# Kernel tuning notes

Hardware: AMD Instinct MI355X
Metric: run time of the kernel (lower is better)

Reference implementation:

```python
import jax, jax.numpy as jnp
import numpy as np

B, N, D = 4096, 32768, 1024

def _l2norm(x, eps=1e-12):
    # matches F.normalize(p=2, dim=-1): x / max(||x||, eps)
    n = jnp.sqrt(jnp.sum(x * x, axis=-1, keepdims=True))
    return x / jnp.maximum(n, eps)

def setup_inputs() -> dict:
    key = jax.random.key(0)
    k1, k2, k3 = jax.random.split(key, 3)
    return {
        "query": jax.random.normal(k1, (B, D), dtype=jnp.float32),
        "keys": jax.random.normal(k2, (N, D), dtype=jnp.float32),
        "values": jax.random.normal(k3, (N, D), dtype=jnp.float32),
    }

def reference(query, keys, values):
    q = _l2norm(query.astype(jnp.float32))          # [B, D]
    k = _l2norm(keys.astype(jnp.float32))           # [N, D]
    v = values.astype(jnp.float32)                  # [N, Dv]
    sim = jnp.einsum('bd,nd->bn', q, k)             # [B, N] cosine similarities
    # torch .var(dim=-1) is unbiased (ddof=1)
    attention_var = jnp.var(sim, axis=-1, ddof=1).mean()
    best = jnp.argmax(sim, axis=-1)                 # [B]
    retrieved = v[best]                             # [B, Dv] gather
    return retrieved, attention_var
```

## Files before the change

### kernel.cpp

```cpp
#include <hip/hip_runtime.h>
#include <math.h>
#include <stdint.h>

#define B_ 4096
#define N_ 32768
#define D_ 1024

#define BM 128
#define BN 128
#define NT 2
#define NCHUNK 128
#define KTOT 32

typedef __attribute__((ext_vector_type(8))) short short8;
typedef __attribute__((ext_vector_type(4))) float f4;
typedef unsigned short u16;

__device__ __forceinline__ u16 bf16_rn(float x) {
    uint32_t u = __float_as_uint(x);
    u += 0x7fffu + ((u >> 16) & 1u);
    return (u16)(u >> 16);
}

__device__ __forceinline__ void split4(f4 v, uint2& hpack, uint2& lpack) {
    u16 h[4], l[4];
    #pragma unroll
    for (int e = 0; e < 4; ++e) {
        float x = v[e];
        u16 hb = bf16_rn(x);
        float hf = __uint_as_float(((uint32_t)hb) << 16);
        h[e] = hb;
        l[e] = bf16_rn(x - hf);
    }
    hpack.x = (uint32_t)h[0] | ((uint32_t)h[1] << 16);
    hpack.y = (uint32_t)h[2] | ((uint32_t)h[3] << 16);
    lpack.x = (uint32_t)l[0] | ((uint32_t)l[1] << 16);
    lpack.y = (uint32_t)l[2] | ((uint32_t)l[3] << 16);
}

__device__ __forceinline__ void g2l16(const void* g, void* l) {
    __builtin_amdgcn_global_load_lds(
        (const __attribute__((address_space(1))) char*)(uintptr_t)g,
        (__attribute__((address_space(3))) char*)(uint32_t)(uintptr_t)l,
        16, 0, 0);
}

__global__ __launch_bounds__(256) void norm_kernel(
    const float* __restrict__ q, const float* __restrict__ k,
    float* __restrict__ invq, float* __restrict__ invk,
    float* __restrict__ out)
{
    const int row = blockIdx.x;
    const int t = threadIdx.x;

    const float* src;
    float* dst;
    if (row < B_) { src = q + (size_t)row * D_;          dst = invq + row; }
    else          { src = k + (size_t)(row - B_) * D_;   dst = invk + (row - B_); }

    float4 v = ((const float4*)src)[t];
    float s = v.x * v.x + v.y * v.y + v.z * v.z + v.w * v.w;

    #pragma unroll
    for (int off = 32; off > 0; off >>= 1)
        s += __shfl_down(s, off);

    __shared__ float red[4];
    if ((t & 63) == 0) red[t >> 6] = s;
    __syncthreads();
    if (t == 0) {
        float tot = red[0] + red[1] + red[2] + red[3];
        *dst = 1.0f / fmaxf(sqrtf(tot), 1e-12f);
        if (row == 0) out[(size_t)B_ * D_] = 0.0f;
    }
}

__global__ __launch_bounds__(256) void split_pack_kernel(
    const float* __restrict__ q, const float* __restrict__ k,
    const float* __restrict__ invq, const float* __restrict__ invk,
    u16* __restrict__ qhi, u16* __restrict__ qlo,
    u16* __restrict__ khi, u16* __restrict__ klo)
{
    const int g = blockIdx.x;
    const int lane = threadIdx.x & 63;
    const int w = threadIdx.x >> 6;

    const float* src; const float* inv;
    u16 *dhi, *dlo; int groups, gg;
    if (g < B_ / 16) { src = q; inv = invq; dhi = qhi; dlo = qlo; groups = B_ / 16; gg = g; }
    else { src = k; inv = invk; dhi = khi; dlo = klo; groups = N_ / 16; gg = g - B_ / 16; }

    const int row = gg * 16 + (lane & 15);
    const float scale = inv[row];
    const int kofs = (lane >> 4) * 8;
    const float* rp = src + (size_t)row * D_;

    #pragma unroll 1
    for (int kt = w; kt < KTOT; kt += 4) {
        f4 v0 = *(const f4*)(rp + kt * 32 + kofs);
        f4 v1 = *(const f4*)(rp + kt * 32 + kofs + 4);
        v0 *= scale; v1 *= scale;
        uint2 h0, l0, h1, l1;
        split4(v0, h0, l0);
        split4(v1, h1, l1);
        const size_t cbase = ((size_t)kt * groups + gg) * 512 + lane * 8;
        uint4 hh = {h0.x, h0.y, h1.x, h1.y};
        uint4 ll = {l0.x, l0.y, l1.x, l1.y};
        *(uint4*)(dhi + cbase) = hh;
        *(uint4*)(dlo + cbase) = ll;
    }
}

__global__ __launch_bounds__(256) void sim_stats_kernel(
    const u16* __restrict__ qhi, const u16* __restrict__ qlo,
    const u16* __restrict__ khi, const u16* __restrict__ klo,
    float* __restrict__ partials)
{
    __shared__ __align__(16) char smem[65536];

    const int tid = threadIdx.x;
    const int lane = tid & 63;
    const int w = tid >> 6;
    const int wm = w >> 1, wn = w & 1;
    const int quad = lane >> 4;
    const int l16 = lane & 15;
    const int mtile = blockIdx.x;
    const int chunk = blockIdx.y;
    const int b0 = mtile * BM;

    const u16* sbase = (w == 0) ? qhi : (w == 1) ? qlo : (w == 2) ? khi : klo;
    const int groups = (w < 2) ? (B_ / 16) : (N_ / 16);

    float (*scan)[68] = (float(*)[68])smem;

    float r_sum = 0.f, r_sq = 0.f, r_m1 = -INFINITY, r_m2 = -INFINITY;
    int r_i1 = 0x7fffffff, r_i2 = 0x7fffffff;

    const f4 zf = {0.f, 0.f, 0.f, 0.f};

    for (int nt = 0; nt < NT; ++nt) {
        const int n0 = chunk * (BN * NT) + nt * BN;
        const int g0 = ((w < 2) ? b0 : n0) >> 4;

        __syncthreads();
        {
            const size_t cb = ((size_t)0 * groups + g0) * 512 + lane * 8;
            char* dst = smem + w * 8192;
            #pragma unroll
            for (int t = 0; t < 8; ++t)
                g2l16(sbase + cb + t * 512, dst + t * 1024);
        }

        f4 acc[4][4];
        #pragma unroll
        for (int i = 0; i < 4; ++i)
            #pragma unroll
            for (int j = 0; j < 4; ++j) acc[i][j] = zf;

        for (int kt = 0; kt < KTOT; ++kt) {
            const int cur = kt & 1;
            __syncthreads();
            if (kt + 1 < KTOT) {
                const size_t cb = ((size_t)(kt + 1) * groups + g0) * 512 + lane * 8;
                char* dst = smem + (1 - cur) * 32768 + w * 8192;
                #pragma unroll
                for (int t = 0; t < 8; ++t)
                    g2l16(sbase + cb + t * 512, dst + t * 1024);
            }
            const char* cbuf = smem + cur * 32768;

            short8 ah[4], al[4];
            #pragma unroll
            for (int i = 0; i < 4; ++i) {
                ah[i] = *(const short8*)(cbuf + (wm * 4 + i) * 1024 + lane * 16);
                al[i] = *(const short8*)(cbuf + 8192 + (wm * 4 + i) * 1024 + lane * 16);
            }
            #pragma unroll
            for (int j = 0; j < 4; ++j) {
                short8 bh = *(const short8*)(cbuf + 16384 + (wn * 4 + j) * 1024 + lane * 16);
                short8 bl = *(const short8*)(cbuf + 24576 + (wn * 4 + j) * 1024 + lane * 16);
                #pragma unroll
                for (int i = 0; i < 4; ++i) {
                    acc[i][j] = __builtin_amdgcn_mfma_f32_16x16x32_bf16(ah[i], bh, acc[i][j], 0, 0, 0);
                    acc[i][j] = __builtin_amdgcn_mfma_f32_16x16x32_bf16(ah[i], bl, acc[i][j], 0, 0, 0);
                    acc[i][j] = __builtin_amdgcn_mfma_f32_16x16x32_bf16(al[i], bh, acc[i][j], 0, 0, 0);
                }
            }
        }

        const int srow = tid >> 1;
        const int c0 = (tid & 1) * 32;
        #pragma unroll 1
        for (int h = 0; h < 2; ++h) {
            __syncthreads();
            if (wn == h) {
                #pragma unroll
                for (int i = 0; i < 4; ++i)
                    #pragma unroll
                    for (int j = 0; j < 4; ++j)
                        #pragma unroll
                        for (int p = 0; p < 4; ++p)
                            scan[wm*64 + i*16 + quad*4 + p][j*16 + l16] = acc[i][j][p];
            }
            __syncthreads();
            const int gbase = n0 + h * 64 + c0;
            #pragma unroll
            for (int u = 0; u < 8; ++u) {
                const f4 v = *(const f4*)&scan[srow][c0 + 4*u];
                #pragma unroll
                for (int e = 0; e < 4; ++e) {
                    const float sv = v[e];
                    const int gi = gbase + 4*u + e;
                    r_sum += sv;
                    r_sq = fmaf(sv, sv, r_sq);
                    if (sv > r_m1)      { r_m2 = r_m1; r_i2 = r_i1; r_m1 = sv; r_i1 = gi; }
                    else if (sv > r_m2) { r_m2 = sv; r_i2 = gi; }
                }
            }
        }
    }

    __syncthreads();
    float* mb = (float*)smem;
    mb[tid*6+0] = r_sum; mb[tid*6+1] = r_sq;
    mb[tid*6+2] = r_m1;  mb[tid*6+3] = __int_as_float(r_i1);
    mb[tid*6+4] = r_m2;  mb[tid*6+5] = __int_as_float(r_i2);
    __syncthreads();
    if ((tid & 1) == 0) {
        const float* o = mb + (size_t)(tid + 1) * 6;
        const float bs = o[0], bq = o[1], bm1 = o[2], bm2 = o[4];
        const int bi1 = __float_as_int(o[3]), bi2 = __float_as_int(o[5]);
        float s = r_sum + bs, q2 = r_sq + bq;
        float m1 = r_m1, m2 = r_m2; int i1 = r_i1, i2 = r_i2;
        if (bm1 > m1 || (bm1 == m1 && bi1 < i1)) {
            float nm2; int ni2;
            if (m1 > bm2 || (m1 == bm2 && i1 < bi2)) { nm2 = m1; ni2 = i1; }
            else                                     { nm2 = bm2; ni2 = bi2; }
            m1 = bm1; i1 = bi1; m2 = nm2; i2 = ni2;
        } else if (bm1 > m2 || (bm1 == m2 && bi1 < i2)) {
            m2 = bm1; i2 = bi1;
        }
        const int row = b0 + (tid >> 1);
        float* p = partials + ((size_t)row * NCHUNK + chunk) * 8;
        f4 p0 = {s, q2, m1, __int_as_float(i1)};
        f4 p1 = {m2, __int_as_float(i2), 0.f, 0.f};
        *(f4*)p = p0;
        *(f4*)(p + 4) = p1;
    }
}

__global__ __launch_bounds__(64) void finalize_kernel(
    const float* __restrict__ partials,
    const float* __restrict__ qg, const float* __restrict__ kg,
    const float* __restrict__ values,
    const float* __restrict__ invq, const float* __restrict__ invk,
    float* __restrict__ out)
{
    const int b = blockIdx.x;
    const int lane = threadIdx.x;

    float s = 0.f, q2 = 0.f, m1 = -INFINITY, m2 = -INFINITY;
    int i1 = 0x7fffffff, i2 = 0x7fffffff;
    #pragma unroll
    for (int cc = 0; cc < NCHUNK / 64; ++cc) {
        const int c = lane + cc * 64;
        const float* p = partials + ((size_t)b * NCHUNK + c) * 8;
        const float bs = p[0], bq = p[1], bm1 = p[2], bm2 = p[4];
        const int bi1 = __float_as_int(p[3]), bi2 = __float_as_int(p[5]);
        s += bs; q2 += bq;
        if (bm1 > m1 || (bm1 == m1 && bi1 < i1)) {
            float nm2; int ni2;
            if (m1 > bm2 || (m1 == bm2 && i1 < bi2)) { nm2 = m1; ni2 = i1; }
            else                                     { nm2 = bm2; ni2 = bi2; }
            m1 = bm1; i1 = bi1; m2 = nm2; i2 = ni2;
        } else if (bm1 > m2 || (bm1 == m2 && bi1 < i2)) {
            m2 = bm1; i2 = bi1;
        }
    }
    #pragma unroll
    for (int msk = 1; msk < 64; msk <<= 1) {
        const float bs = __shfl_xor(s, msk), bq = __shfl_xor(q2, msk);
        const float bm1 = __shfl_xor(m1, msk), bm2 = __shfl_xor(m2, msk);
        const int bi1 = __shfl_xor(i1, msk), bi2 = __shfl_xor(i2, msk);
        s += bs; q2 += bq;
        if (bm1 > m1 || (bm1 == m1 && bi1 < i1)) {
            float nm2; int ni2;
            if (m1 > bm2 || (m1 == bm2 && i1 < bi2)) { nm2 = m1; ni2 = i1; }
            else                                     { nm2 = bm2; ni2 = bi2; }
            m1 = bm1; i1 = bi1; m2 = nm2; i2 = ni2;
        } else if (bm1 > m2 || (bm1 == m2 && bi1 < i2)) {
            m2 = bm1; i2 = bi1;
        }
    }
    if (lane == 0) {
        const float var = (q2 - s * s / (float)N_) / (float)(N_ - 1);
        atomicAdd(out + (size_t)B_ * D_, var * (1.0f / B_));
    }

    const float* qrow = qg + (size_t)b * D_;
    const float* k1 = kg + (size_t)i1 * D_;
    const float* k2 = kg + (size_t)i2 * D_;
    double d1 = 0.0, d2 = 0.0;
    #pragma unroll
    for (int v4 = 0; v4 < 4; ++v4) {
        const int off = v4 * 256 + lane * 4;
        const f4 qv = *(const f4*)(qrow + off);
        const f4 a1 = *(const f4*)(k1 + off);
        const f4 a2 = *(const f4*)(k2 + off);
        #pragma unroll
        for (int e = 0; e < 4; ++e) {
            d1 += (double)qv[e] * (double)a1[e];
            d2 += (double)qv[e] * (double)a2[e];
        }
    }
    #pragma unroll
    for (int msk = 1; msk < 64; msk <<= 1) {
        d1 += __shfl_xor(d1, msk);
        d2 += __shfl_xor(d2, msk);
    }
    const double sc = (double)invq[b];
    const double s1 = d1 * sc * (double)invk[i1];
    const double s2 = d2 * sc * (double)invk[i2];
    const int winner = (s2 > s1 || (s2 == s1 && i2 < i1)) ? i2 : i1;

    const float* vrow = values + (size_t)winner * D_;
    float* orow = out + (size_t)b * D_;
    #pragma unroll
    for (int v4 = 0; v4 < 4; ++v4) {
        const int off = v4 * 256 + lane * 4;
        *(f4*)(orow + off) = *(const f4*)(vrow + off);
    }
}

extern "C" void kernel_launch(void* const* d_in, const int* in_sizes, int n_in,
                              void* d_out, int out_size, void* d_ws, size_t ws_size,
                              hipStream_t stream)
{
    const float* q = (const float*)d_in[0];
    const float* k = (const float*)d_in[1];
    const float* v = (const float*)d_in[2];
    float* out = (float*)d_out;
    float* ws = (float*)d_ws;

    float* invq = ws;
    float* invk = ws + B_;
    float* partials = ws + B_ + N_;
    u16* qhi = (u16*)(partials + (size_t)B_ * NCHUNK * 8);
    u16* qlo = qhi + (size_t)B_ * D_;
    u16* khi = qlo + (size_t)B_ * D_;
    u16* klo = khi + (size_t)N_ * D_;

    norm_kernel<<<B_ + N_, 256, 0, stream>>>(q, k, invq, invk, out);
    split_pack_kernel<<<(B_ + N_) / 16, 256, 0, stream>>>(q, k, invq, invk, qhi, qlo, khi, klo);
    sim_stats_kernel<<<dim3(B_ / BM, NCHUNK), 256, 0, stream>>>(qhi, qlo, khi, klo, partials);
    finalize_kernel<<<B_, 64, 0, stream>>>(partials, q, k, v, invq, invk, out);
}
```

Measured before the change: 1.006 ms.

## Fuse norm into pack kernel and load Q fragments directly from global

Merges the row-norm kernel into the split/pack kernel so each row is read once and one launch disappears. In the similarity kernel, the A (query) fragments are now loaded straight from global memory into registers instead of being staged through LDS. This halves the shared-memory buffer and adds a launch-bounds occupancy hint of 4 blocks. The risk is exposed global-load latency on the A operand each k-step, since only B stays double-buffered.

```diff
diff --git a/kernel.cpp b/kernel.cpp
--- a/kernel.cpp
+++ b/kernel.cpp
@@ -11,6 +11,8 @@
 #define NT 2
 #define NCHUNK 128
 #define KTOT 32
+#define QG (B_ / 16)
+#define KG (N_ / 16)
 
 typedef __attribute__((ext_vector_type(8))) short short8;
 typedef __attribute__((ext_vector_type(4))) float f4;
@@ -45,78 +47,71 @@
         16, 0, 0);
 }
 
-__global__ __launch_bounds__(256) void norm_kernel(
+__global__ __launch_bounds__(256) void pack_kernel(
     const float* __restrict__ q, const float* __restrict__ k,
     float* __restrict__ invq, float* __restrict__ invk,
+    u16* __restrict__ qhi, u16* __restrict__ qlo,
+    u16* __restrict__ khi, u16* __restrict__ klo,
     float* __restrict__ out)
-{
-    const int row = blockIdx.x;
-    const int t = threadIdx.x;
-
-    const float* src;
-    float* dst;
-    if (row < B_) { src = q + (size_t)row * D_;          dst = invq + row; }
-    else          { src = k + (size_t)(row - B_) * D_;   dst = invk + (row - B_); }
-
-    float4 v = ((const float4*)src)[t];
-    float s = v.x * v.x + v.y * v.y + v.z * v.z + v.w * v.w;
-
-    #pragma unroll
-    for (int off = 32; off > 0; off >>= 1)
-        s += __shfl_down(s, off);
-
-    __shared__ float red[4];
-    if ((t & 63) == 0) red[t >> 6] = s;
-    __syncthreads();
-    if (t == 0) {
-        float tot = red[0] + red[1] + red[2] + red[3];
-        *dst = 1.0f / fmaxf(sqrtf(tot), 1e-12f);
-        if (row == 0) out[(size_t)B_ * D_] = 0.0f;
-    }
-}
-
-__global__ __launch_bounds__(256) void split_pack_kernel(
-    const float* __restrict__ q, const float* __restrict__ k,
-    const float* __restrict__ invq, const float* __restrict__ invk,
-    u16* __restrict__ qhi, u16* __restrict__ qlo,
-    u16* __restrict__ khi, u16* __restrict__ klo)
 {
     const int g = blockIdx.x;
     const int lane = threadIdx.x & 63;
     const int w = threadIdx.x >> 6;
 
-    const float* src; const float* inv;
+    const float* src; float* invdst;
     u16 *dhi, *dlo; int groups, gg;
-    if (g < B_ / 16) { src = q; inv = invq; dhi = qhi; dlo = qlo; groups = B_ / 16; gg = g; }
-    else { src = k; inv = invk; dhi = khi; dlo = klo; groups = N_ / 16; gg = g - B_ / 16; }
+    if (g < B_ / 16) { src = q; invdst = invq; dhi = qhi; dlo = qlo; groups = QG; gg = g; }
+    else { src = k; invdst = invk; dhi = khi; dlo = klo; groups = KG; gg = g - B_ / 16; }
 
     const int row = gg * 16 + (lane & 15);
-    const float scale = inv[row];
     const int kofs = (lane >> 4) * 8;
     const float* rp = src + (size_t)row * D_;
 
-    #pragma unroll 1
-    for (int kt = w; kt < KTOT; kt += 4) {
-        f4 v0 = *(const f4*)(rp + kt * 32 + kofs);
-        f4 v1 = *(const f4*)(rp + kt * 32 + kofs + 4);
-        v0 *= scale; v1 *= scale;
+    f4 v0[8], v1[8];
+    float s = 0.f;
+    #pragma unroll
+    for (int u = 0; u < 8; ++u) {
+        const int kt = w + u * 4;
+        v0[u] = *(const f4*)(rp + kt * 32 + kofs);
+        v1[u] = *(const f4*)(rp + kt * 32 + kofs + 4);
+        #pragma unroll
+        for (int e = 0; e < 4; ++e) {
+            s = fmaf(v0[u][e], v0[u][e], s);
+            s = fmaf(v1[u][e], v1[u][e], s);
+        }
+    }
+    s += __shfl_xor(s, 16);
+    s += __shfl_xor(s, 32);
+    __shared__ float red[4][16];
+    if ((lane >> 4) == 0) red[w][lane & 15] = s;
+    __syncthreads();
+    const float tot = red[0][lane & 15] + red[1][lane & 15]
+                    + red[2][lane & 15] + red[3][lane & 15];
+    const float scale = 1.0f / fmaxf(sqrtf(tot), 1e-12f);
+    if (w == 0 && lane < 16) invdst[gg * 16 + lane] = scale;
+
+    #pragma unroll
+    for (int u = 0; u < 8; ++u) {
+        const int kt = w + u * 4;
+        f4 a = v0[u] * scale, b = v1[u] * scale;
         uint2 h0, l0, h1, l1;
-        split4(v0, h0, l0);
-        split4(v1, h1, l1);
+        split4(a, h0, l0);
+        split4(b, h1, l1);
         const size_t cbase = ((size_t)kt * groups + gg) * 512 + lane * 8;
         uint4 hh = {h0.x, h0.y, h1.x, h1.y};
         uint4 ll = {l0.x, l0.y, l1.x, l1.y};
         *(uint4*)(dhi + cbase) = hh;
         *(uint4*)(dlo + cbase) = ll;
     }
-}
-
-__global__ __launch_bounds__(256) void sim_stats_kernel(
+    if (g == 0 && threadIdx.x == 0) out[(size_t)B_ * D_] = 0.0f;
+}
+
+__global__ __launch_bounds__(256, 4) void sim_stats_kernel(
     const u16* __restrict__ qhi, const u16* __restrict__ qlo,
     const u16* __restrict__ khi, const u16* __restrict__ klo,
     float* __restrict__ partials)
 {
-    __shared__ __align__(16) char smem[65536];
+    __shared__ __align__(16) char smem[34816];
 
     const int tid = threadIdx.x;
     const int lane = tid & 63;
@@ -128,8 +123,11 @@
     const int chunk = blockIdx.y;
     const int b0 = mtile * BM;
 
-    const u16* sbase = (w == 0) ? qhi : (w == 1) ? qlo : (w == 2) ? khi : klo;
-    const int groups = (w < 2) ? (B_ / 16) : (N_ / 16);
+    const int aG0 = (b0 >> 4) + wm * 4;
+    const int plane = w >> 1;
+    const u16* __restrict__ kbase = plane ? klo : khi;
+    const int sub0 = (w & 1) * 4;
+    char* const dst0 = smem + plane * 8192 + sub0 * 1024;
 
     float (*scan)[68] = (float(*)[68])smem;
 
@@ -140,15 +138,14 @@
 
     for (int nt = 0; nt < NT; ++nt) {
         const int n0 = chunk * (BN * NT) + nt * BN;
-        const int g0 = ((w < 2) ? b0 : n0) >> 4;
+        const int g0 = n0 >> 4;
 
         __syncthreads();
         {
-            const size_t cb = ((size_t)0 * groups + g0) * 512 + lane * 8;
-            char* dst = smem + w * 8192;
+            const size_t cb = ((size_t)(g0 + sub0)) * 512 + lane * 8;
             #pragma unroll
-            for (int t = 0; t < 8; ++t)
-                g2l16(sbase + cb + t * 512, dst + t * 1024);
+            for (int t = 0; t < 4; ++t)
+                g2l16(kbase + cb + t * 512, dst0 + t * 1024);
         }
 
         f4 acc[4][4];
@@ -160,25 +157,30 @@
         for (int kt = 0; kt < KTOT; ++kt) {
             const int cur = kt & 1;
             __syncthreads();
+
+            short8 ah[4], al[4];
+            {
+                const size_t ab = ((size_t)kt * QG + aG0) * 512 + lane * 8;
+                #pragma unroll
+                for (int i = 0; i < 4; ++i) {
+                    ah[i] = *(const short8*)(qhi + ab + i * 512);
+                    al[i] = *(const short8*)(qlo + ab + i * 512);
+                }
+            }
+
             if (kt + 1 < KTOT) {
-                const size_t cb = ((size_t)(kt + 1) * groups + g0) * 512 + lane * 8;
-                char* dst = smem + (1 - cur) * 32768 + w * 8192;
-                #pragma unroll
-                for (int t = 0; t < 8; ++t)
-                    g2l16(sbase + cb + t * 512, dst + t * 1024);
-            }
-            const char* cbuf = smem + cur * 32768;
-
-            short8 ah[4], al[4];
-            #pragma unroll
-            for (int i = 0; i < 4; ++i) {
-                ah[i] = *(const short8*)(cbuf + (wm * 4 + i) * 1024 + lane * 16);
-                al[i] = *(const short8*)(cbuf + 8192 + (wm * 4 + i) * 1024 + lane * 16);
-            }
+                const size_t cb = ((size_t)(kt + 1) * KG + g0 + sub0) * 512 + lane * 8;
+                char* dst = smem + (1 - cur) * 16384 + plane * 8192 + sub0 * 1024;
+                #pragma unroll
+                for (int t = 0; t < 4; ++t)
+                    g2l16(kbase + cb + t * 512, dst + t * 1024);
+            }
+
+            const char* cbuf = smem + cur * 16384;
             #pragma unroll
             for (int j = 0; j < 4; ++j) {
-                short8 bh = *(const short8*)(cbuf + 16384 + (wn * 4 + j) * 1024 + lane * 16);
-                short8 bl = *(const short8*)(cbuf + 24576 + (wn * 4 + j) * 1024 + lane * 16);
+                short8 bh = *(const short8*)(cbuf + (wn * 4 + j) * 1024 + lane * 16);
+                short8 bl = *(const short8*)(cbuf + 8192 + (wn * 4 + j) * 1024 + lane * 16);
                 #pragma unroll
                 for (int i = 0; i < 4; ++i) {
                     acc[i][j] = __builtin_amdgcn_mfma_f32_16x16x32_bf16(ah[i], bh, acc[i][j], 0, 0, 0);
@@ -350,8 +352,7 @@
     u16* khi = qlo + (size_t)B_ * D_;
     u16* klo = khi + (size_t)N_ * D_;
 
-    norm_kernel<<<B_ + N_, 256, 0, stream>>>(q, k, invq, invk, out);
-    split_pack_kernel<<<(B_ + N_) / 16, 256, 0, stream>>>(q, k, invq, invk, qhi, qlo, khi, klo);
+    pack_kernel<<<(B_ + N_) / 16, 256, 0, stream>>>(q, k, invq, invk, qhi, qlo, khi, klo, out);
     sim_stats_kernel<<<dim3(B_ / BM, NCHUNK), 256, 0, stream>>>(qhi, qlo, khi, klo, partials);
     finalize_kernel<<<B_, 64, 0, stream>>>(partials, q, k, v, invq, invk, out);
 }
```

Measured after the change: 1.020 ms. No clear change (+1.4%).
